# Kernel optimization log

Measured on AMD Instinct MI355X. Metric: run time of the kernel, lower is better.

## Reference

```python
import jax, jax.numpy as jnp
import numpy as np

B, D, G, N = 256, 512, 64, 8   # batch, latent_dim, num_on_states, n_states
K = G * N                      # total codebook entries


def setup_inputs() -> dict:
    key = jax.random.key(0)
    k1, k2, k3, k4 = jax.random.split(key, 4)
    input_mu = jax.random.normal(k1, (B, D), dtype=jnp.float32)
    input_logsig = 0.5 * jax.random.normal(k2, (B, D), dtype=jnp.float32)
    # codebook init, matching the torch module: mus ~ 3*N(0,1), sigs ~ 3*exp(2*N(0,1))
    on_mus = 3.0 * jax.random.normal(k3, (K, D), dtype=jnp.float32)
    on_sigs = 3.0 * jnp.exp(2.0 * jax.random.normal(k4, (K, D), dtype=jnp.float32))
    on_states = jnp.stack([on_mus, on_sigs], axis=-1)  # [K, D, 2]
    return {"input_mu": input_mu, "input_logsig": input_logsig, "on_states": on_states}


def _w2_sq_all(input_mu, input_sig, mus, sigs):
    """Squared 2-Wasserstein dist between diag Gaussians, for all (codebook k, batch b).
    Returns [K, B] = ||mu_k - mu_b||^2 + ||sig_k - sig_b||^2, via the expanded form
    so the whole per-entry python loop collapses into two GEMMs."""
    d = (jnp.sum(mus**2, -1)[:, None] + jnp.sum(input_mu**2, -1)[None, :]
         - 2.0 * mus @ input_mu.T)
    d = d + (jnp.sum(sigs**2, -1)[:, None] + jnp.sum(input_sig**2, -1)[None, :]
             - 2.0 * sigs @ input_sig.T)
    return d


def reference(input_mu, input_logsig, on_states):
    # mode is fixed to 'softmin' (the differentiable branch of the torch module)
    Bv = input_mu.shape[0]
    input_sig = jnp.exp(input_logsig)
    mus, sigs = on_states[:, :, 0], on_states[:, :, 1]          # [K, D] each

    d_kb = _w2_sq_all(input_mu, input_sig, mus, sigs)           # [K, B]
    # faithful to torch: torch.stack(dists).view(B, -1) reshapes [K,B] -> [B,K]
    dists = d_kb.reshape(Bv, -1)                                # [B, K]

    dists_g = dists.reshape(Bv, G, N)                           # contiguous groups of n_states
    softs = jax.nn.softmax(-dists_g, axis=2)                    # F.softmin over each group
    # weighted combination of (mu, sigma) states per group
    states = jnp.einsum('bgn,gnde->bgde', softs, on_states.reshape(G, N, D, 2))  # [B,G,D,2]
    dists_bg = jnp.sum(softs * dists_g, axis=2)                 # [B, G]

    # final soft assignment: F.softmin(dists, dim=0) -> softmax over the BATCH axis (faithful)
    ps = jax.nn.softmax(-dists_bg, axis=0)                      # [B, G]
    # torch.matmul(ps[B,G], states[B,G,D]) broadcasts ps -> result [B, B, D]
    quantised_mu = jnp.einsum('bg,xgd->xbd', ps, states[..., 0])   # [B, B, D]
    quantised_sig = jnp.einsum('bg,xgd->xbd', ps, states[..., 1])  # [B, B, D]
    dist = jnp.sum(dists_bg * ps, axis=1)                       # [B]
    return ((quantised_mu, quantised_sig), dists_bg, dist)
```

## Files before the change

kernel.cpp:

```cpp
#include <hip/hip_runtime.h>
#include <cstddef>
#include <cstdint>

typedef short bf16x8 __attribute__((ext_vector_type(8)));
typedef float f32x4 __attribute__((ext_vector_type(4)));

#define Bsz 256
#define Dsz 512
#define Gsz 64
#define Ksz 512

#define WS_DFLAT 0
#define WS_SOFTS 131072
#define WS_BNORM 278528
#define WS_CNORM 278784
#define WS_PSB   279296
#define WS_ONB   287488
#define WS_ZB    549632

#define ONB_STRIDE 262144
#define ZB_STRIDE  131072

#define OUT_QMU  0
#define OUT_QSIG 33554432
#define OUT_DBG  67108864
#define OUT_DIST 67125248

__device__ __forceinline__ unsigned short f2bf(float f) {
  unsigned int u = __float_as_uint(f);
  u = (u + 0x7FFFu + ((u >> 16) & 1u)) >> 16;
  return (unsigned short)u;
}
__device__ __forceinline__ float bf2f(unsigned short h) {
  return __uint_as_float(((unsigned int)h) << 16);
}

__global__ __launch_bounds__(256) void k_prep(const float* __restrict__ mu,
                                              const float* __restrict__ ls,
                                              const float* __restrict__ on,
                                              float* __restrict__ ws) {
  int t = threadIdx.x;
  __shared__ float red[256];
  if (blockIdx.x < 512) {
    int k = blockIdx.x;
    float4 v = *(const float4*)(on + (size_t)k * 1024 + 4 * t);
    unsigned short* onb0 = (unsigned short*)(ws + WS_ONB);
    unsigned short* onb1 = onb0 + ONB_STRIDE;
    *(ushort2*)&onb0[(size_t)k * 512 + 2 * t] = make_ushort2(f2bf(v.x), f2bf(v.z));
    *(ushort2*)&onb1[(size_t)k * 512 + 2 * t] = make_ushort2(f2bf(v.y), f2bf(v.w));
    red[t] = v.x * v.x + v.y * v.y + v.z * v.z + v.w * v.w;
    __syncthreads();
    for (int off = 128; off > 0; off >>= 1) {
      if (t < off) red[t] += red[t + off];
      __syncthreads();
    }
    if (t == 0) ws[WS_CNORM + k] = red[0];
  } else {
    int b = blockIdx.x - 512;
    unsigned short* zb0 = (unsigned short*)(ws + WS_ZB);
    unsigned short* zb1 = zb0 + ZB_STRIDE;
    float part = 0.f;
    for (int d = t; d < Dsz; d += 256) {
      float m = mu[b * Dsz + d];
      float s = expf(ls[b * Dsz + d]);
      zb0[(size_t)b * 512 + d] = f2bf(m);
      zb1[(size_t)b * 512 + d] = f2bf(s);
      part += m * m + s * s;
    }
    red[t] = part;
    __syncthreads();
    for (int off = 128; off > 0; off >>= 1) {
      if (t < off) red[t] += red[t + off];
      __syncthreads();
    }
    if (t == 0) ws[WS_BNORM + b] = red[0];
  }
}

__global__ __launch_bounds__(256) void k_dkb(float* __restrict__ ws,
                                             float* __restrict__ out) {
  __shared__ float pl[4][16][33];
  int t = threadIdx.x, l = t & 63, w = t >> 6;
  int lr = l & 15, lh = l >> 4;
  if (blockIdx.x == 0) out[OUT_DIST + t] = 0.f;
  int kt = blockIdx.x >> 3, bt = blockIdx.x & 7;
  int k0 = kt * 16, b0 = bt * 32;
  const unsigned short* Ap =
      (const unsigned short*)(ws + WS_ONB) + (size_t)(w >> 1) * ONB_STRIDE + (size_t)k0 * 512;
  const unsigned short* Bp =
      (const unsigned short*)(ws + WS_ZB) + (size_t)(w >> 1) * ZB_STRIDE + (size_t)b0 * 512;
  int dbase = (w & 1) * 256;

  f32x4 acc[2];
#pragma unroll
  for (int j = 0; j < 2; ++j) { acc[j][0] = 0.f; acc[j][1] = 0.f; acc[j][2] = 0.f; acc[j][3] = 0.f; }

#pragma unroll
  for (int kk = 0; kk < 8; ++kk) {
    int dl = dbase + kk * 32 + lh * 8;
    bf16x8 a0 = *(const bf16x8*)(Ap + (size_t)lr * 512 + dl);
    bf16x8 q0 = *(const bf16x8*)(Bp + (size_t)lr * 512 + dl);
    bf16x8 q1 = *(const bf16x8*)(Bp + (size_t)(lr + 16) * 512 + dl);
    acc[0] = __builtin_amdgcn_mfma_f32_16x16x32_bf16(a0, q0, acc[0], 0, 0, 0);
    acc[1] = __builtin_amdgcn_mfma_f32_16x16x32_bf16(a0, q1, acc[1], 0, 0, 0);
  }

#pragma unroll
  for (int j = 0; j < 2; ++j)
#pragma unroll
    for (int r = 0; r < 4; ++r)
      pl[w][lh * 4 + r][j * 16 + lr] = acc[j][r];
  __syncthreads();

  int r = t >> 4, c = (t & 15) * 2;
  float s0 = pl[0][r][c] + pl[1][r][c] + pl[2][r][c] + pl[3][r][c];
  float s1 = pl[0][r][c + 1] + pl[1][r][c + 1] + pl[2][r][c + 1] + pl[3][r][c + 1];
  float cn = ws[WS_CNORM + k0 + r];
  float2 o = make_float2(cn + ws[WS_BNORM + b0 + c] - 2.f * s0,
                         cn + ws[WS_BNORM + b0 + c + 1] - 2.f * s1);
  *(float2*)&ws[WS_DFLAT + (size_t)(k0 + r) * 256 + b0 + c] = o;
}

__global__ __launch_bounds__(256) void k_sm(float* __restrict__ ws,
                                            float* __restrict__ out) {
  int g = blockIdx.x, t = threadIdx.x;
  const float* df = ws + WS_DFLAT;
  int k = 2 * t + (g >> 5);
  int col = (g & 31) << 3;
  const float* p = df + (size_t)k * 256 + col;
  float4 v0 = *(const float4*)p;
  float4 v1 = *(const float4*)(p + 4);
  float d[8] = {v0.x, v0.y, v0.z, v0.w, v1.x, v1.y, v1.z, v1.w};
  float m = d[0];
#pragma unroll
  for (int n = 1; n < 8; ++n) m = fminf(m, d[n]);
  float wv[8], s = 0.f, wd = 0.f;
#pragma unroll
  for (int n = 0; n < 8; ++n) {
    wv[n] = expf(m - d[n]);
    s += wv[n];
    wd += wv[n] * d[n];
  }
  float inv = 1.f / s;
  float* so = ws + WS_SOFTS + (size_t)t * 512 + g * 8;
  *(float4*)so = make_float4(wv[0] * inv, wv[1] * inv, wv[2] * inv, wv[3] * inv);
  *(float4*)(so + 4) = make_float4(wv[4] * inv, wv[5] * inv, wv[6] * inv, wv[7] * inv);
  float dbg = wd * inv;
  out[OUT_DBG + t * 64 + g] = dbg;

  __shared__ float red[256];
  red[t] = dbg;
  __syncthreads();
  for (int off = 128; off > 0; off >>= 1) {
    if (t < off) red[t] = fminf(red[t], red[t + off]);
    __syncthreads();
  }
  float mm = red[0];
  __syncthreads();
  float wp = expf(mm - dbg);
  red[t] = wp;
  __syncthreads();
  for (int off = 128; off > 0; off >>= 1) {
    if (t < off) red[t] += red[t + off];
    __syncthreads();
  }
  float psv = wp / red[0];
  ((unsigned short*)(ws + WS_PSB))[t * 64 + g] = f2bf(psv);
  atomicAdd(&out[OUT_DIST + t], psv * dbg);
}

__global__ __launch_bounds__(256) void k_quant(const float* __restrict__ ws,
                                               float* __restrict__ out) {
  __shared__ __align__(16) unsigned short psl[16384];
  __shared__ __align__(16) unsigned short st[2][4096];
  __shared__ float sxl[576];
  int x = blockIdx.x >> 3, dt = blockIdx.x & 7;
  int dBase = dt * 64;
  int t = threadIdx.x, l = t & 63, w = t >> 6;
  int lr = l & 15, lh = l >> 4;

  const unsigned short* psb = (const unsigned short*)(ws + WS_PSB);
#pragma unroll
  for (int c = 0; c < 8; ++c) {
    int cc = t + c * 256;
    int b = cc >> 3, gw8 = (cc & 7) * 8;
    bf16x8 v = *(const bf16x8*)(psb + (size_t)b * 64 + gw8);
    *(bf16x8*)&psl[(b * 64 + gw8) ^ ((b & 7) << 3)] = v;
  }
  {
    int i0 = t, i1 = t + 256;
    sxl[(i0 >> 3) * 9 + (i0 & 7)] = ws[WS_SOFTS + (size_t)x * 512 + i0];
    sxl[(i1 >> 3) * 9 + (i1 & 7)] = ws[WS_SOFTS + (size_t)x * 512 + i1];
  }
  __syncthreads();

  int dq = t & 15, gq = t >> 4;
#pragma unroll 1
  for (int e = 0; e < 2; ++e) {
    const unsigned short* ob =
        (const unsigned short*)(ws + WS_ONB) + (size_t)e * ONB_STRIDE + dBase + dq * 4;
    float av[4][4];
#pragma unroll
    for (int gg = 0; gg < 4; ++gg) {
      int g = gq * 4 + gg;
      float a0 = 0.f, a1 = 0.f, a2 = 0.f, a3 = 0.f;
      const unsigned short* rp = ob + (size_t)(g * 8) * 512;
#pragma unroll
      for (int n = 0; n < 8; ++n) {
        ushort4 vv = *(const ushort4*)(rp + (size_t)n * 512);
        float swv = sxl[g * 9 + n];
        a0 += swv * bf2f(vv.x);
        a1 += swv * bf2f(vv.y);
        a2 += swv * bf2f(vv.z);
        a3 += swv * bf2f(vv.w);
      }
      av[gg][0] = a0; av[gg][1] = a1; av[gg][2] = a2; av[gg][3] = a3;
    }
#pragma unroll
    for (int dd = 0; dd < 4; ++dd) {
      int d = dq * 4 + dd;
      ushort4 o = make_ushort4(f2bf(av[0][dd]), f2bf(av[1][dd]), f2bf(av[2][dd]), f2bf(av[3][dd]));
      *(ushort4*)&st[e][(d * 64 + gq * 4) ^ ((d & 7) << 3)] = o;
    }
  }
  __syncthreads();

  bf16x8 bn[4][2];
#pragma unroll
  for (int j = 0; j < 4; ++j)
#pragma unroll
    for (int kk = 0; kk < 2; ++kk) {
      int b = w * 64 + j * 16 + lr;
      bn[j][kk] = *(const bf16x8*)&psl[(b * 64 + kk * 32 + lh * 8) ^ ((b & 7) << 3)];
    }

#pragma unroll 1
  for (int e = 0; e < 2; ++e) {
    bf16x8 am[4][2];
#pragma unroll
    for (int i = 0; i < 4; ++i)
#pragma unroll
      for (int kk = 0; kk < 2; ++kk)
        am[i][kk] = *(const bf16x8*)&st[e][((i * 16 + lr) * 64 + kk * 32 + lh * 8) ^ ((lr & 7) << 3)];

    f32x4 acc[4][4];
#pragma unroll
    for (int i = 0; i < 4; ++i)
#pragma unroll
      for (int j = 0; j < 4; ++j) {
        acc[i][j][0] = 0.f; acc[i][j][1] = 0.f; acc[i][j][2] = 0.f; acc[i][j][3] = 0.f;
      }
#pragma unroll
    for (int kk = 0; kk < 2; ++kk)
#pragma unroll
      for (int i = 0; i < 4; ++i)
#pragma unroll
        for (int j = 0; j < 4; ++j)
          acc[i][j] = __builtin_amdgcn_mfma_f32_16x16x32_bf16(am[i][kk], bn[j][kk], acc[i][j], 0, 0, 0);

    float* op = out + (e ? (size_t)OUT_QSIG : (size_t)OUT_QMU) + (size_t)x * (256 * 512);
#pragma unroll
    for (int i = 0; i < 4; ++i)
#pragma unroll
      for (int j = 0; j < 4; ++j) {
        size_t off = (size_t)(w * 64 + j * 16 + lr) * 512 + dBase + i * 16 + lh * 4;
        *(f32x4*)&op[off] = acc[i][j];
      }
  }
}

extern "C" void kernel_launch(void* const* d_in, const int* in_sizes, int n_in,
                              void* d_out, int out_size, void* d_ws, size_t ws_size,
                              hipStream_t stream) {
  (void)in_sizes; (void)n_in; (void)out_size; (void)ws_size;
  const float* mu = (const float*)d_in[0];
  const float* ls = (const float*)d_in[1];
  const float* on = (const float*)d_in[2];
  float* out = (float*)d_out;
  float* ws = (float*)d_ws;

  k_prep<<<dim3(768), dim3(256), 0, stream>>>(mu, ls, on, ws);
  k_dkb<<<dim3(256), dim3(256), 0, stream>>>(ws, out);
  k_sm<<<dim3(64), dim3(256), 0, stream>>>(ws, out);
  k_quant<<<dim3(2048), dim3(256), 0, stream>>>(ws, out);
}
```

Before: 75.30 us.

## Process two x rows per k_quant block and stream MFMA output per column tile

k_quant now launches 1024 blocks of 512 threads, and each half-block handles a different x row. The bf16 ps tile in shared memory is loaded once and shared by both rows, which halves the redundant ps staging per output. The MFMA stage now loops over j one tile at a time. It loads B fragments on the fly and stores each 4-tile result immediately instead of holding a 4x4 accumulator array, which lowers register pressure to improve occupancy. The cost is more LDS reads of ps per j and a non-unrolled loop that may serialize the stores.

Measured after the change: 79.77 us. 1.06x slower.

```diff
diff --git a/kernel.cpp b/kernel.cpp
--- a/kernel.cpp
+++ b/kernel.cpp
@@ -169,32 +169,35 @@
   atomicAdd(&out[OUT_DIST + t], psv * dbg);
 }
 
-__global__ __launch_bounds__(256) void k_quant(const float* __restrict__ ws,
+__global__ __launch_bounds__(512) void k_quant(const float* __restrict__ ws,
                                                float* __restrict__ out) {
   __shared__ __align__(16) unsigned short psl[16384];
-  __shared__ __align__(16) unsigned short st[2][4096];
-  __shared__ float sxl[576];
-  int x = blockIdx.x >> 3, dt = blockIdx.x & 7;
+  __shared__ __align__(16) unsigned short st[2][2][4096];
+  __shared__ float sxl[2][576];
+  int xp = blockIdx.x >> 3, dt = blockIdx.x & 7;
   int dBase = dt * 64;
-  int t = threadIdx.x, l = t & 63, w = t >> 6;
+  int t = threadIdx.x;
+  int h = t >> 8, t2 = t & 255;
+  int x = xp * 2 + h;
+  int l = t & 63, w4 = (t >> 6) & 3;
   int lr = l & 15, lh = l >> 4;
 
   const unsigned short* psb = (const unsigned short*)(ws + WS_PSB);
 #pragma unroll
-  for (int c = 0; c < 8; ++c) {
-    int cc = t + c * 256;
+  for (int c = 0; c < 4; ++c) {
+    int cc = t + c * 512;
     int b = cc >> 3, gw8 = (cc & 7) * 8;
     bf16x8 v = *(const bf16x8*)(psb + (size_t)b * 64 + gw8);
     *(bf16x8*)&psl[(b * 64 + gw8) ^ ((b & 7) << 3)] = v;
   }
   {
-    int i0 = t, i1 = t + 256;
-    sxl[(i0 >> 3) * 9 + (i0 & 7)] = ws[WS_SOFTS + (size_t)x * 512 + i0];
-    sxl[(i1 >> 3) * 9 + (i1 & 7)] = ws[WS_SOFTS + (size_t)x * 512 + i1];
-  }
-  __syncthreads();
-
-  int dq = t & 15, gq = t >> 4;
+    int i0 = t2, i1 = t2 + 256;
+    sxl[h][(i0 >> 3) * 9 + (i0 & 7)] = ws[WS_SOFTS + (size_t)x * 512 + i0];
+    sxl[h][(i1 >> 3) * 9 + (i1 & 7)] = ws[WS_SOFTS + (size_t)x * 512 + i1];
+  }
+  __syncthreads();
+
+  int dq = t2 & 15, gq = t2 >> 4;
 #pragma unroll 1
   for (int e = 0; e < 2; ++e) {
     const unsigned short* ob =
@@ -208,7 +211,7 @@
 #pragma unroll
       for (int n = 0; n < 8; ++n) {
         ushort4 vv = *(const ushort4*)(rp + (size_t)n * 512);
-        float swv = sxl[g * 9 + n];
+        float swv = sxl[h][g * 9 + n];
         a0 += swv * bf2f(vv.x);
         a1 += swv * bf2f(vv.y);
         a2 += swv * bf2f(vv.z);
@@ -220,19 +223,10 @@
     for (int dd = 0; dd < 4; ++dd) {
       int d = dq * 4 + dd;
       ushort4 o = make_ushort4(f2bf(av[0][dd]), f2bf(av[1][dd]), f2bf(av[2][dd]), f2bf(av[3][dd]));
-      *(ushort4*)&st[e][(d * 64 + gq * 4) ^ ((d & 7) << 3)] = o;
-    }
-  }
-  __syncthreads();
-
-  bf16x8 bn[4][2];
-#pragma unroll
-  for (int j = 0; j < 4; ++j)
-#pragma unroll
-    for (int kk = 0; kk < 2; ++kk) {
-      int b = w * 64 + j * 16 + lr;
-      bn[j][kk] = *(const bf16x8*)&psl[(b * 64 + kk * 32 + lh * 8) ^ ((b & 7) << 3)];
-    }
+      *(ushort4*)&st[h][e][(d * 64 + gq * 4) ^ ((d & 7) << 3)] = o;
+    }
+  }
+  __syncthreads();
 
 #pragma unroll 1
   for (int e = 0; e < 2; ++e) {
@@ -241,31 +235,29 @@
     for (int i = 0; i < 4; ++i)
 #pragma unroll
       for (int kk = 0; kk < 2; ++kk)
-        am[i][kk] = *(const bf16x8*)&st[e][((i * 16 + lr) * 64 + kk * 32 + lh * 8) ^ ((lr & 7) << 3)];
-
-    f32x4 acc[4][4];
-#pragma unroll
-    for (int i = 0; i < 4; ++i)
-#pragma unroll
-      for (int j = 0; j < 4; ++j) {
-        acc[i][j][0] = 0.f; acc[i][j][1] = 0.f; acc[i][j][2] = 0.f; acc[i][j][3] = 0.f;
+        am[i][kk] =
+            *(const bf16x8*)&st[h][e][((i * 16 + lr) * 64 + kk * 32 + lh * 8) ^ ((lr & 7) << 3)];
+
+    float* op = out + (e ? (size_t)OUT_QSIG : (size_t)OUT_QMU) + (size_t)x * (256 * 512);
+#pragma unroll 1
+    for (int j = 0; j < 4; ++j) {
+      int b = w4 * 64 + j * 16 + lr;
+      bf16x8 b0 = *(const bf16x8*)&psl[(b * 64 + lh * 8) ^ ((b & 7) << 3)];
+      bf16x8 b1 = *(const bf16x8*)&psl[(b * 64 + 32 + lh * 8) ^ ((b & 7) << 3)];
+      f32x4 a4[4];
+#pragma unroll
+      for (int i = 0; i < 4; ++i) { a4[i][0] = 0.f; a4[i][1] = 0.f; a4[i][2] = 0.f; a4[i][3] = 0.f; }
+#pragma unroll
+      for (int i = 0; i < 4; ++i) {
+        a4[i] = __builtin_amdgcn_mfma_f32_16x16x32_bf16(am[i][0], b0, a4[i], 0, 0, 0);
+        a4[i] = __builtin_amdgcn_mfma_f32_16x16x32_bf16(am[i][1], b1, a4[i], 0, 0, 0);
       }
 #pragma unroll
-    for (int kk = 0; kk < 2; ++kk)
-#pragma unroll
-      for (int i = 0; i < 4; ++i)
-#pragma unroll
-        for (int j = 0; j < 4; ++j)
-          acc[i][j] = __builtin_amdgcn_mfma_f32_16x16x32_bf16(am[i][kk], bn[j][kk], acc[i][j], 0, 0, 0);
-
-    float* op = out + (e ? (size_t)OUT_QSIG : (size_t)OUT_QMU) + (size_t)x * (256 * 512);
-#pragma unroll
-    for (int i = 0; i < 4; ++i)
-#pragma unroll
-      for (int j = 0; j < 4; ++j) {
-        size_t off = (size_t)(w * 64 + j * 16 + lr) * 512 + dBase + i * 16 + lh * 4;
-        *(f32x4*)&op[off] = acc[i][j];
+      for (int i = 0; i < 4; ++i) {
+        size_t off = (size_t)(w4 * 64 + j * 16 + lr) * 512 + dBase + i * 16 + lh * 4;
+        *(f32x4*)&op[off] = a4[i];
       }
+    }
   }
 }
 
@@ -282,5 +274,5 @@
   k_prep<<<dim3(768), dim3(256), 0, stream>>>(mu, ls, on, ws);
   k_dkb<<<dim3(256), dim3(256), 0, stream>>>(ws, out);
   k_sm<<<dim3(64), dim3(256), 0, stream>>>(ws, out);
-  k_quant<<<dim3(2048), dim3(256), 0, stream>>>(ws, out);
-}
+  k_quant<<<dim3(1024), dim3(512), 0, stream>>>(ws, out);
+}
```
